# Kernel tuning notes

Hardware: AMD Instinct MI355X
Metric: run time of the kernel (lower is better)

Reference implementation:

```python
import jax, jax.numpy as jnp
import numpy as np

B, H, W, C, NB = 3, 256, 256, 16, 4
EPS = 1e-3  # keras BatchNormalization default epsilon


def _conv(x, w, b):
    y = jax.lax.conv_general_dilated(x, w, (1, 1), 'SAME',
                                     dimension_numbers=('NHWC', 'HWIO', 'NHWC'))
    return y + b


def _bn(x, g, be, mu, v):
    # inference-mode batch norm with moving statistics
    return (x - mu) * jax.lax.rsqrt(v + EPS) * g + be


def _extract_patches(x, p, s):
    # tf.image.extract_patches(..., padding='SAME') -> (b, oh, ow, p, p, c)
    b, h, w, c = x.shape
    oh, ow = -(-h // s), -(-w // s)
    pth = max((oh - 1) * s + p - h, 0)
    ptw = max((ow - 1) * s + p - w, 0)
    xp = jnp.pad(x, ((0, 0), (pth // 2, pth - pth // 2), (ptw // 2, ptw - ptw // 2), (0, 0)))
    ri = np.arange(oh)[:, None] * s + np.arange(p)[None, :]  # (oh, p)
    ci = np.arange(ow)[:, None] * s + np.arange(p)[None, :]  # (ow, p)
    return xp[:, ri[:, None, :, None], ci[None, :, None, :], :]


def setup_inputs() -> dict:
    key = jax.random.key(0)
    ks = jax.random.split(key, 4)
    mr = jax.random.normal(ks[0], (B, H, W, C), jnp.float32)
    pet = jax.random.normal(ks[1], (B, H, W, C), jnp.float32)
    W1 = jax.random.normal(ks[2], (3, 3, C, C * NB), jnp.float32) * 0.05
    W2 = jax.random.normal(ks[3], (3, 3, C * NB, C * NB), jnp.float32) * 0.05
    z = jnp.zeros((C * NB,), jnp.float32)
    o = jnp.ones((C * NB,), jnp.float32)
    return dict(mr_features=mr, pet_features=pet,
                W1=W1, b1=z, g1=o, be1=z, mu1=z, v1=o,
                W2=W2, b2=z, g2=o, be2=z, mu2=z, v2=o,
                patch=8, stride=4)


def reference(mr_features, pet_features, W1, b1, g1, be1, mu1, v1,
              W2, b2, g2, be2, mu2, v2, patch, stride):
    px = py = int(patch)
    sx = sy = int(stride)
    bsz, h, w, c = mr_features.shape

    # ---- B_Kernel_Function_Generator ----
    x = jax.nn.relu(_bn(_conv(mr_features, W1, b1), g1, be1, mu1, v1))
    x = _bn(_conv(x, W2, b2), g2, be2, mu2, v2)  # last conv_block: no activation
    nb = x.shape[-1] // c
    x = x.reshape(bsz, h, w, c, nb)
    x = jax.nn.softmax(x, axis=-1)
    b_features = jnp.where(x > 1e-5, x, 0.0)  # mask * x

    # ---- Sparse_Kernel_Matrix_Multiplication ----
    bc, bf = c, nb
    Nx, Ny = h // px, w // py
    lx, ly = px // sx, py // sy
    SNx, SNy = Nx * lx, Ny * ly

    bflat = b_features.reshape(bsz, h, w, bc * bf)
    bp = _extract_patches(bflat, px, sx).reshape(bsz, SNx, SNy, px, py, bc, bf)
    pp = _extract_patches(pet_features, px, sx).reshape(bsz, SNx, SNy, px, py, bc, 1)

    dn = jnp.sum(bp, axis=(3, 4), keepdims=True)              # diagonal norm
    kp = jnp.sum(pp * bp, axis=(3, 4), keepdims=True)         # kernel-weighted PET
    dn_safe = jnp.where(dn == 0, 1.0, dn)
    kn = jnp.where(dn == 0, 0.0, kp / dn_safe) * bp           # divide_no_nan
    kpet = jnp.sum(kn, axis=-1)                               # (b,SNx,SNy,px,py,bc)

    # deinterleave stride phases: kernel_pet[:, i::lx, j::ly] stack
    kp6 = kpet.reshape(bsz, Nx, lx, Ny, ly, px, py, c)
    st = kp6.transpose(4, 2, 0, 1, 3, 5, 6, 7).reshape(lx * ly, bsz, Nx, Ny, px, py, c)
    t = st.transpose(1, 2, 3, 4, 5, 6, 0).reshape(bsz, Nx, Ny, px, py, c, lx, ly)
    t = t.transpose(0, 1, 3, 2, 4, 5, 6, 7).reshape(bsz, Nx * px, Ny * py, c, lx, ly)
    t = t.transpose(4, 5, 0, 1, 2, 3)  # (lx, ly, b, H, W, c)

    # align_patches: roll each shifted copy back into registration, then mean
    rev = t.transpose(2, 3, 4, 5, 0, 1).reshape(bsz, h, w, c, lx * ly)
    rev = rev.transpose(4, 0, 1, 2, 3)  # (lx*ly, b, H, W, c)
    rollx = np.arange(-px // 2 + sx // 2, px // 2 + sx // 2, sx)
    rolly = np.arange(-py // 2 + sy // 2, py // 2 + sy // 2, sy)
    acc = jnp.zeros((bsz, h, w, c), rev.dtype)
    for m in range(lx * ly):  # small fixed set (lx*ly = 4)
        acc = acc + jnp.roll(rev[m], (int(rollx[m % lx]), int(rolly[m // lx])), axis=(1, 2))
    return acc / (lx * ly)
```

## Files before the change

### kernel.cpp

```cpp
#include <hip/hip_runtime.h>

#define EPSB 1e-3f

typedef _Float16 half8 __attribute__((ext_vector_type(8)));
typedef _Float16 half4 __attribute__((ext_vector_type(4)));
typedef float f32x4 __attribute__((ext_vector_type(4)));

__global__ __launch_bounds__(256, 4)
void k_prep(const float* __restrict__ W1, const float* __restrict__ W2,
            const float* __restrict__ b1, const float* __restrict__ g1,
            const float* __restrict__ be1, const float* __restrict__ mu1,
            const float* __restrict__ v1,
            const float* __restrict__ b2, const float* __restrict__ g2,
            const float* __restrict__ be2, const float* __restrict__ mu2,
            const float* __restrict__ v2,
            _Float16* __restrict__ W1F, _Float16* __restrict__ W2F,
            float* __restrict__ ST)
{
    int t = blockIdx.x * 256 + threadIdx.x;
    if (t < 5 * 4 * 64 * 8) {
        int k = t & 7, lane = (t >> 3) & 63, snt = t >> 9;
        int s = snt >> 2, ct = snt & 3;
        int quad = lane >> 4, n16 = lane & 15;
        int tap = 2 * s + (quad >> 1);
        int ci  = (quad & 1) * 8 + k;
        int co  = ct * 16 + n16;
        float v = (tap < 9) ? W1[(tap * 16 + ci) * 64 + co] : 0.f;
        W1F[t] = (_Float16)v;
        return;
    }
    t -= 5 * 4 * 64 * 8;
    if (t < 18 * 4 * 64 * 8) {
        int k = t & 7, lane = (t >> 3) & 63, snt = t >> 9;
        int s = snt >> 2, ct = snt & 3;
        int quad = lane >> 4, n16 = lane & 15;
        int tap = s >> 1;
        int ci  = (s & 1) * 32 + quad * 8 + k;
        int co  = ct * 16 + n16;
        W2F[t] = (_Float16)W2[(tap * 64 + ci) * 64 + co];
        return;
    }
    t -= 18 * 4 * 64 * 8;
    if (t < 256) {
        int c = t & 63, sel = t >> 6;
        if (sel == 0)      ST[c]       = g1[c] * rsqrtf(v1[c] + EPSB);
        else if (sel == 1) ST[64 + c]  = (b1[c] - mu1[c]) * (g1[c] * rsqrtf(v1[c] + EPSB)) + be1[c];
        else if (sel == 2) ST[128 + c] = g2[c] * rsqrtf(v2[c] + EPSB);
        else               ST[192 + c] = (b2[c] - mu2[c]) * (g2[c] * rsqrtf(v2[c] + EPSB)) + be2[c];
    }
}

#define CIP1 24
__global__ __launch_bounds__(256, 2)
void k_conv1(const float* __restrict__ mr, const _Float16* __restrict__ W1F,
             const float* __restrict__ ST, _Float16* __restrict__ A)
{
    __shared__ __align__(16) _Float16 sIn[6 * 66 * CIP1];
    const int tid = threadIdx.x;
    const int b  = blockIdx.y;
    const int r0 = (blockIdx.x >> 2) * 4;
    const int q0 = (blockIdx.x & 3) * 64;

    for (int idx = tid; idx < 6 * 66 * 2; idx += 256) {
        int c = idx & 1, pp = idx >> 1;
        int p = pp % 66, dy = pp / 66;
        int rr = r0 + dy - 1, qg = q0 + p - 1;
        half8 h = (half8)(_Float16)0.f;
        if ((unsigned)rr < 256u && (unsigned)qg < 256u) {
            const float* src = mr + ((b * 256 + rr) * 256 + qg) * 16 + c * 8;
            float4 v0 = *(const float4*)src;
            float4 v1 = *(const float4*)(src + 4);
            h = (half8){(_Float16)v0.x, (_Float16)v0.y, (_Float16)v0.z, (_Float16)v0.w,
                        (_Float16)v1.x, (_Float16)v1.y, (_Float16)v1.z, (_Float16)v1.w};
        }
        *(half8*)(&sIn[(dy * 66 + p) * CIP1 + c * 8]) = h;
    }
    __syncthreads();

    const int w = tid >> 6, lane = tid & 63;
    const int n16 = lane & 15, quad = lane >> 4;
    const int ci0 = (quad & 1) * 8;

    f32x4 acc[4][4];
    #pragma unroll
    for (int i = 0; i < 4; ++i)
        #pragma unroll
        for (int j = 0; j < 4; ++j) acc[i][j] = (f32x4){0.f, 0.f, 0.f, 0.f};

    #pragma unroll
    for (int s = 0; s < 5; ++s) {
        int tap  = 2 * s + (quad >> 1);
        int tapc = tap > 8 ? 8 : tap;
        int dy = tapc / 3, dx = tapc % 3;
        half8 wfrag[4], pfrag[4];
        #pragma unroll
        for (int ct = 0; ct < 4; ++ct)
            wfrag[ct] = *(const half8*)(W1F + ((s * 4 + ct) * 64 + lane) * 8);
        #pragma unroll
        for (int qt = 0; qt < 4; ++qt)
            pfrag[qt] = *(const half8*)&sIn[((w + dy) * 66 + qt * 16 + n16 + dx) * CIP1 + ci0];
        #pragma unroll
        for (int qt = 0; qt < 4; ++qt)
            #pragma unroll
            for (int ct = 0; ct < 4; ++ct)
                acc[qt][ct] = __builtin_amdgcn_mfma_f32_16x16x32_f16(wfrag[ct], pfrag[qt], acc[qt][ct], 0, 0, 0);
    }

    const int r = r0 + w;
    #pragma unroll
    for (int ct = 0; ct < 4; ++ct) {
        int co0 = ct * 16 + quad * 4;
        f32x4 sc = *(const f32x4*)&ST[co0];
        f32x4 sh = *(const f32x4*)&ST[64 + co0];
        #pragma unroll
        for (int qt = 0; qt < 4; ++qt) {
            int q = q0 + qt * 16 + n16;
            half4 h;
            #pragma unroll
            for (int j = 0; j < 4; ++j)
                h[j] = (_Float16)fmaxf(acc[qt][ct][j] * sc[j] + sh[j], 0.f);
            *(half4*)(A + (((b * 256 + r) * 256 + q) * 64 + co0)) = h;
        }
    }
}

#define CIP2 72
__global__ __launch_bounds__(256, 2)
void k_conv2(const _Float16* __restrict__ A, const _Float16* __restrict__ W2F,
             const float* __restrict__ ST, _Float16* __restrict__ BF)
{
    __shared__ __align__(16) _Float16 sIn[6 * 66 * CIP2];
    const int tid = threadIdx.x;
    const int b  = blockIdx.y;
    const int r0 = (blockIdx.x >> 2) * 4;
    const int q0 = (blockIdx.x & 3) * 64;

    for (int idx = tid; idx < 6 * 66 * 8; idx += 256) {
        int c = idx & 7, pp = idx >> 3;
        int p = pp % 66, dy = pp / 66;
        int rr = r0 + dy - 1, qg = q0 + p - 1;
        int4 v = {0, 0, 0, 0};
        if ((unsigned)rr < 256u && (unsigned)qg < 256u)
            v = *(const int4*)(A + (((b * 256 + rr) * 256 + qg) * 64 + c * 8));
        *(int4*)(&sIn[(dy * 66 + p) * CIP2 + c * 8]) = v;
    }
    __syncthreads();

    const int w = tid >> 6, lane = tid & 63;
    const int n16 = lane & 15, quad = lane >> 4;

    f32x4 acc[4][4];
    #pragma unroll
    for (int i = 0; i < 4; ++i)
        #pragma unroll
        for (int j = 0; j < 4; ++j) acc[i][j] = (f32x4){0.f, 0.f, 0.f, 0.f};

    #pragma unroll
    for (int s = 0; s < 18; ++s) {
        const int tap = s >> 1;
        const int dy = tap / 3, dx = tap % 3;
        const int ci0 = (s & 1) * 32 + quad * 8;
        half8 wfrag[4], pfrag[4];
        #pragma unroll
        for (int ct = 0; ct < 4; ++ct)
            wfrag[ct] = *(const half8*)(W2F + ((s * 4 + ct) * 64 + lane) * 8);
        #pragma unroll
        for (int qt = 0; qt < 4; ++qt)
            pfrag[qt] = *(const half8*)&sIn[((w + dy) * 66 + qt * 16 + n16 + dx) * CIP2 + ci0];
        #pragma unroll
        for (int qt = 0; qt < 4; ++qt)
            #pragma unroll
            for (int ct = 0; ct < 4; ++ct)
                acc[qt][ct] = __builtin_amdgcn_mfma_f32_16x16x32_f16(wfrag[ct], pfrag[qt], acc[qt][ct], 0, 0, 0);
    }

    const int r = r0 + w;
    #pragma unroll
    for (int ct = 0; ct < 4; ++ct) {
        int co0 = ct * 16 + quad * 4;
        f32x4 sc = *(const f32x4*)&ST[128 + co0];
        f32x4 sh = *(const f32x4*)&ST[192 + co0];
        #pragma unroll
        for (int qt = 0; qt < 4; ++qt) {
            int q = q0 + qt * 16 + n16;
            float z0 = acc[qt][ct][0] * sc[0] + sh[0];
            float z1 = acc[qt][ct][1] * sc[1] + sh[1];
            float z2 = acc[qt][ct][2] * sc[2] + sh[2];
            float z3 = acc[qt][ct][3] * sc[3] + sh[3];
            float mx = fmaxf(fmaxf(z0, z1), fmaxf(z2, z3));
            float e0 = __expf(z0 - mx), e1 = __expf(z1 - mx);
            float e2 = __expf(z2 - mx), e3 = __expf(z3 - mx);
            float inv = __builtin_amdgcn_rcpf((e0 + e1) + (e2 + e3));
            float p0 = e0 * inv, p1 = e1 * inv, p2 = e2 * inv, p3 = e3 * inv;
            half4 h;
            h[0] = (_Float16)(p0 > 1e-5f ? p0 : 0.f);
            h[1] = (_Float16)(p1 > 1e-5f ? p1 : 0.f);
            h[2] = (_Float16)(p2 > 1e-5f ? p2 : 0.f);
            h[3] = (_Float16)(p3 > 1e-5f ? p3 : 0.f);
            *(half4*)(BF + (((b * 256 + r) * 256 + q) * 64 + co0)) = h;
        }
    }
}

__global__ __launch_bounds__(256, 4)
void k_s2(const _Float16* __restrict__ BF, const float* __restrict__ pet,
          float* __restrict__ S2)
{
    int t = blockIdx.x * 256 + threadIdx.x;
    int c8 = t & 7;
    int q2 = (t >> 3) & 127;
    int r2 = (t >> 10) & 127;
    int b  = t >> 17;
    float dn[8], kp[8];
    #pragma unroll
    for (int k = 0; k < 8; ++k) { dn[k] = 0.f; kp[k] = 0.f; }
    #pragma unroll
    for (int u = 0; u < 2; ++u)
        #pragma unroll
        for (int v = 0; v < 2; ++v) {
            int rr = 2 * r2 + u, qq = 2 * q2 + v;
            half8 bf = *(const half8*)(BF + (((b * 256 + rr) * 256 + qq) * 64 + c8 * 8));
            float2 pv = *(const float2*)(pet + ((b * 256 + rr) * 256 + qq) * 16 + c8 * 2);
            #pragma unroll
            for (int k = 0; k < 8; ++k) {
                float bv = (float)bf[k];
                dn[k] += bv;
                kp[k] = fmaf(k < 4 ? pv.x : pv.y, bv, kp[k]);
            }
        }
    float* o = S2 + 2 * ((size_t)((b * 128 + r2) * 128 + q2) * 64 + c8 * 8);
    #pragma unroll
    for (int k = 0; k < 4; ++k)
        *(float4*)(o + 4 * k) = make_float4(dn[2*k], kp[2*k], dn[2*k+1], kp[2*k+1]);
}

__global__ __launch_bounds__(256, 4)
void k_ratio(const float* __restrict__ S2, float* __restrict__ RATIO)
{
    int t = blockIdx.x * 256 + threadIdx.x;
    int cf = t & 63;
    int j  = (t >> 6) & 63;
    int i  = (t >> 12) & 63;
    int b  = t >> 18;
    float dn = 0.f, kp = 0.f;
    #pragma unroll
    for (int u = 0; u < 4; ++u) {
        int r2 = 2 * i - 1 + u;
        if ((unsigned)r2 >= 128u) continue;
        #pragma unroll
        for (int v = 0; v < 4; ++v) {
            int q2 = 2 * j - 1 + v;
            if ((unsigned)q2 >= 128u) continue;
            float2 s = *(const float2*)(S2 + 2 * (((b * 128 + r2) * 128 + q2) * 64 + cf));
            dn += s.x;
            kp += s.y;
        }
    }
    RATIO[t] = (dn == 0.f) ? 0.f : kp * __builtin_amdgcn_rcpf(dn);
}

__global__ __launch_bounds__(256, 4)
void k_out(const _Float16* __restrict__ BF, const float* __restrict__ RATIO,
           float* __restrict__ out)
{
    int tid = blockIdx.x * 256 + threadIdx.x;
    int c = tid & 15;
    int q = (tid >> 4) & 255;
    int r = (tid >> 12) & 255;
    int b = tid >> 20;
    int i0 = (r <= 253) ? (((r + 2) >> 3) << 1)        : -1;
    int i1 = (r >= 2)   ? ((((r - 2) >> 3) << 1) | 1)  : -1;
    int j0 = (q <= 253) ? (((q + 2) >> 3) << 1)        : -1;
    int j1 = (q >= 2)   ? ((((q - 2) >> 3) << 1) | 1)  : -1;
    float Sx = 0.f, Sy = 0.f, Sz = 0.f, Sw = 0.f;
    const float* Rb = &RATIO[(size_t)b * 64 * 64 * 64 + 4 * c];
    #pragma unroll
    for (int pi = 0; pi < 2; ++pi) {
        int ii = pi ? i1 : i0;
        if (ii < 0) continue;
        #pragma unroll
        for (int pj = 0; pj < 2; ++pj) {
            int jj = pj ? j1 : j0;
            if (jj < 0) continue;
            float4 r4 = *(const float4*)&Rb[(ii * 64 + jj) * 64];
            Sx += r4.x; Sy += r4.y; Sz += r4.z; Sw += r4.w;
        }
    }
    half4 bf4 = *(const half4*)(BF + (size_t)tid * 4);
    out[tid] = 0.25f * ((float)bf4[0] * Sx + (float)bf4[1] * Sy +
                        (float)bf4[2] * Sz + (float)bf4[3] * Sw);
}

extern "C" void kernel_launch(void* const* d_in, const int* in_sizes, int n_in,
                              void* d_out, int out_size, void* d_ws, size_t ws_size,
                              hipStream_t stream) {
    const float* mr  = (const float*)d_in[0];
    const float* pet = (const float*)d_in[1];
    const float* W1  = (const float*)d_in[2];
    const float* b1  = (const float*)d_in[3];
    const float* g1  = (const float*)d_in[4];
    const float* be1 = (const float*)d_in[5];
    const float* mu1 = (const float*)d_in[6];
    const float* v1  = (const float*)d_in[7];
    const float* W2  = (const float*)d_in[8];
    const float* b2  = (const float*)d_in[9];
    const float* g2  = (const float*)d_in[10];
    const float* be2 = (const float*)d_in[11];
    const float* mu2 = (const float*)d_in[12];
    const float* v2  = (const float*)d_in[13];

    char* ws = (char*)d_ws;
    _Float16* A     = (_Float16*)(ws);
    _Float16* BF    = (_Float16*)(ws + 25165824);
    float*    S2    = (float*)(ws + 50331648);
    float*    RATIO = (float*)(ws + 75497472);
    _Float16* W1F   = (_Float16*)(ws + 78643200);
    _Float16* W2F   = (_Float16*)(ws + 78663680);
    float*    ST    = (float*)(ws + 78737408);
    float*    out   = (float*)d_out;

    dim3 blk(256);
    k_prep<<<185, blk, 0, stream>>>(W1, W2, b1, g1, be1, mu1, v1,
                                    b2, g2, be2, mu2, v2, W1F, W2F, ST);
    k_conv1<<<dim3(256, 3), blk, 0, stream>>>(mr, W1F, ST, A);
    k_conv2<<<dim3(256, 3), blk, 0, stream>>>(A, W2F, ST, BF);
    k_s2<<<1536, blk, 0, stream>>>(BF, pet, S2);
    k_ratio<<<3072, blk, 0, stream>>>(S2, RATIO);
    k_out<<<12288, blk, 0, stream>>>(BF, RATIO, out);
}
```

Before: 177.7 us.

## Fuse 2x2 pooling into conv2 epilogue and tile output kernel via shared ratios

Measured after the change: 177.1 us. Within noise of the previous version (-0.3%).

```diff
diff --git a/kernel.cpp b/kernel.cpp
--- a/kernel.cpp
+++ b/kernel.cpp
@@ -51,7 +51,7 @@
 }
 
 #define CIP1 24
-__global__ __launch_bounds__(256, 2)
+__global__ __launch_bounds__(256, 3)
 void k_conv1(const float* __restrict__ mr, const _Float16* __restrict__ W1F,
              const float* __restrict__ ST, _Float16* __restrict__ A)
 {
@@ -127,7 +127,8 @@
 #define CIP2 72
 __global__ __launch_bounds__(256, 2)
 void k_conv2(const _Float16* __restrict__ A, const _Float16* __restrict__ W2F,
-             const float* __restrict__ ST, _Float16* __restrict__ BF)
+             const float* __restrict__ ST, const float* __restrict__ pet,
+             _Float16* __restrict__ BF, float* __restrict__ S2)
 {
     __shared__ __align__(16) _Float16 sIn[6 * 66 * CIP2];
     const int tid = threadIdx.x;
@@ -175,6 +176,7 @@
     }
 
     const int r = r0 + w;
+    half4 hv[4][4];
     #pragma unroll
     for (int ct = 0; ct < 4; ++ct) {
         int co0 = ct * 16 + quad * 4;
@@ -197,41 +199,54 @@
             h[1] = (_Float16)(p1 > 1e-5f ? p1 : 0.f);
             h[2] = (_Float16)(p2 > 1e-5f ? p2 : 0.f);
             h[3] = (_Float16)(p3 > 1e-5f ? p3 : 0.f);
+            hv[ct][qt] = h;
             *(half4*)(BF + (((b * 256 + r) * 256 + q) * 64 + co0)) = h;
         }
     }
-}
-
-__global__ __launch_bounds__(256, 4)
-void k_s2(const _Float16* __restrict__ BF, const float* __restrict__ pet,
-          float* __restrict__ S2)
-{
-    int t = blockIdx.x * 256 + threadIdx.x;
-    int c8 = t & 7;
-    int q2 = (t >> 3) & 127;
-    int r2 = (t >> 10) & 127;
-    int b  = t >> 17;
-    float dn[8], kp[8];
-    #pragma unroll
-    for (int k = 0; k < 8; ++k) { dn[k] = 0.f; kp[k] = 0.f; }
+
+    __syncthreads();
+    #pragma unroll
+    for (int ct = 0; ct < 4; ++ct) {
+        int co0 = ct * 16 + quad * 4;
+        #pragma unroll
+        for (int qt = 0; qt < 4; ++qt) {
+            int ql = qt * 16 + n16;
+            *(half4*)(&sIn[(w * 64 + ql) * CIP2 + co0]) = hv[ct][qt];
+        }
+    }
+    __syncthreads();
+
+    const int k4 = tid & 3;
+    const int cell = tid >> 2;
+    const int rp = cell >> 5, qp = cell & 31;
+    float dn[16], kp[16];
+    #pragma unroll
+    for (int j = 0; j < 16; ++j) { dn[j] = 0.f; kp[j] = 0.f; }
     #pragma unroll
     for (int u = 0; u < 2; ++u)
         #pragma unroll
         for (int v = 0; v < 2; ++v) {
-            int rr = 2 * r2 + u, qq = 2 * q2 + v;
-            half8 bf = *(const half8*)(BF + (((b * 256 + rr) * 256 + qq) * 64 + c8 * 8));
-            float2 pv = *(const float2*)(pet + ((b * 256 + rr) * 256 + qq) * 16 + c8 * 2);
-            #pragma unroll
-            for (int k = 0; k < 8; ++k) {
-                float bv = (float)bf[k];
-                dn[k] += bv;
-                kp[k] = fmaf(k < 4 ? pv.x : pv.y, bv, kp[k]);
+            int rl = 2 * rp + u, ql = 2 * qp + v;
+            half8 b0 = *(const half8*)(&sIn[(rl * 64 + ql) * CIP2 + k4 * 16]);
+            half8 b1 = *(const half8*)(&sIn[(rl * 64 + ql) * CIP2 + k4 * 16 + 8]);
+            float4 p4 = *(const float4*)(pet + ((b * 256 + r0 + rl) * 256 + q0 + ql) * 16 + 4 * k4);
+            #pragma unroll
+            for (int j = 0; j < 8; ++j) {
+                float bv = (float)b0[j];
+                dn[j] += bv;
+                kp[j] = fmaf((j < 4) ? p4.x : p4.y, bv, kp[j]);
             }
-        }
-    float* o = S2 + 2 * ((size_t)((b * 128 + r2) * 128 + q2) * 64 + c8 * 8);
-    #pragma unroll
-    for (int k = 0; k < 4; ++k)
-        *(float4*)(o + 4 * k) = make_float4(dn[2*k], kp[2*k], dn[2*k+1], kp[2*k+1]);
+            #pragma unroll
+            for (int j = 0; j < 8; ++j) {
+                float bv = (float)b1[j];
+                dn[8 + j] += bv;
+                kp[8 + j] = fmaf((j < 4) ? p4.z : p4.w, bv, kp[8 + j]);
+            }
+        }
+    float* o = S2 + 2 * ((size_t)(((b * 128 + (r0 >> 1) + rp) * 128 + (q0 >> 1) + qp) * 64) + 16 * k4);
+    #pragma unroll
+    for (int m = 0; m < 8; ++m)
+        *(float4*)(o + 4 * m) = make_float4(dn[2*m], kp[2*m], dn[2*m+1], kp[2*m+1]);
 }
 
 __global__ __launch_bounds__(256, 4)
@@ -256,39 +271,65 @@
             kp += s.y;
         }
     }
-    RATIO[t] = (dn == 0.f) ? 0.f : kp * __builtin_amdgcn_rcpf(dn);
+    RATIO[t] = (dn == 0.f) ? 0.f : 0.25f * kp * __builtin_amdgcn_rcpf(dn);
 }
 
 __global__ __launch_bounds__(256, 4)
 void k_out(const _Float16* __restrict__ BF, const float* __restrict__ RATIO,
            float* __restrict__ out)
 {
-    int tid = blockIdx.x * 256 + threadIdx.x;
-    int c = tid & 15;
-    int q = (tid >> 4) & 255;
-    int r = (tid >> 12) & 255;
-    int b = tid >> 20;
-    int i0 = (r <= 253) ? (((r + 2) >> 3) << 1)        : -1;
-    int i1 = (r >= 2)   ? ((((r - 2) >> 3) << 1) | 1)  : -1;
-    int j0 = (q <= 253) ? (((q + 2) >> 3) << 1)        : -1;
-    int j1 = (q >= 2)   ? ((((q - 2) >> 3) << 1) | 1)  : -1;
-    float Sx = 0.f, Sy = 0.f, Sz = 0.f, Sw = 0.f;
-    const float* Rb = &RATIO[(size_t)b * 64 * 64 * 64 + 4 * c];
-    #pragma unroll
-    for (int pi = 0; pi < 2; ++pi) {
-        int ii = pi ? i1 : i0;
-        if (ii < 0) continue;
-        #pragma unroll
-        for (int pj = 0; pj < 2; ++pj) {
-            int jj = pj ? j1 : j0;
-            if (jj < 0) continue;
-            float4 r4 = *(const float4*)&Rb[(ii * 64 + jj) * 64];
-            Sx += r4.x; Sy += r4.y; Sz += r4.z; Sw += r4.w;
-        }
-    }
-    half4 bf4 = *(const half4*)(BF + (size_t)tid * 4);
-    out[tid] = 0.25f * ((float)bf4[0] * Sx + (float)bf4[1] * Sy +
-                        (float)bf4[2] * Sz + (float)bf4[3] * Sw);
+    __shared__ __align__(16) float sR[2 * 64 * 68];
+    const int tid = threadIdx.x;
+    const int r = blockIdx.x & 255;
+    const int b = blockIdx.x >> 8;
+
+    const int i0 = (r <= 253) ? 2 * ((r + 2) >> 3)       : -1;
+    const int i1 = (r >= 2)   ? 2 * ((r - 2) >> 3) + 1   : -1;
+
+    for (int idx = tid; idx < 2048; idx += 256) {
+        int ph = idx >> 10, rest = idx & 1023;
+        int j = rest >> 4, c4 = rest & 15;
+        int ii = ph ? i1 : i0;
+        float4 v = make_float4(0.f, 0.f, 0.f, 0.f);
+        if (ii >= 0)
+            v = *(const float4*)&RATIO[(((b * 64 + ii) * 64 + j) << 6) + 4 * c4];
+        *(float4*)&sR[(ph * 64 + j) * 68 + 4 * c4] = v;
+    }
+    __syncthreads();
+
+    const int q = tid;
+    const int j0 = (q <= 253) ? 2 * ((q + 2) >> 3)     : -1;
+    const int j1 = (q >= 2)   ? 2 * ((q - 2) >> 3) + 1 : -1;
+
+    const half8* bfp = (const half8*)(BF + ((size_t)(b * 256 + r) * 256 + q) * 64);
+    float o[16];
+    #pragma unroll
+    for (int c = 0; c < 16; ++c) o[c] = 0.f;
+
+    #pragma unroll
+    for (int c2 = 0; c2 < 8; ++c2) {
+        half8 bf8 = bfp[c2];
+        float s0 = 0.f, s1 = 0.f;
+        #pragma unroll
+        for (int pi = 0; pi < 2; ++pi) {
+            #pragma unroll
+            for (int pj = 0; pj < 2; ++pj) {
+                int jj = pj ? j1 : j0;
+                if (jj < 0) continue;
+                const float* rp_ = &sR[(pi * 64 + jj) * 68 + 8 * c2];
+                s0 += (float)bf8[0] * rp_[0] + (float)bf8[1] * rp_[1]
+                    + (float)bf8[2] * rp_[2] + (float)bf8[3] * rp_[3];
+                s1 += (float)bf8[4] * rp_[4] + (float)bf8[5] * rp_[5]
+                    + (float)bf8[6] * rp_[6] + (float)bf8[7] * rp_[7];
+            }
+        }
+        o[2 * c2]     = s0;
+        o[2 * c2 + 1] = s1;
+    }
+    float* op = out + ((size_t)(b * 256 + r) * 256 + q) * 16;
+    #pragma unroll
+    for (int m = 0; m < 4; ++m)
+        *(float4*)(op + 4 * m) = make_float4(o[4*m], o[4*m+1], o[4*m+2], o[4*m+3]);
 }
 
 extern "C" void kernel_launch(void* const* d_in, const int* in_sizes, int n_in,
@@ -323,8 +364,7 @@
     k_prep<<<185, blk, 0, stream>>>(W1, W2, b1, g1, be1, mu1, v1,
                                     b2, g2, be2, mu2, v2, W1F, W2F, ST);
     k_conv1<<<dim3(256, 3), blk, 0, stream>>>(mr, W1F, ST, A);
-    k_conv2<<<dim3(256, 3), blk, 0, stream>>>(A, W2F, ST, BF);
-    k_s2<<<1536, blk, 0, stream>>>(BF, pet, S2);
+    k_conv2<<<dim3(256, 3), blk, 0, stream>>>(A, W2F, ST, pet, BF, S2);
     k_ratio<<<3072, blk, 0, stream>>>(S2, RATIO);
-    k_out<<<12288, blk, 0, stream>>>(BF, RATIO, out);
-}
+    k_out<<<768, blk, 0, stream>>>(BF, RATIO, out);
+}
```
